# Performance work log

Measured on AMD Instinct MI355X. Metric: run time of the kernel, lower is better.

The kernel has to match this reference:

```python
import jax, jax.numpy as jnp
import numpy as np

B, S, D, H = 4, 2048, 1024, 16
DH = D // H


def setup_inputs() -> dict:
    key = jax.random.key(0)
    ks = jax.random.split(key, 7)
    return {
        "Q": jax.random.normal(ks[0], (B, S, D), dtype=jnp.float32),
        "K": jax.random.normal(ks[1], (B, S, D), dtype=jnp.float32),
        "V": jax.random.normal(ks[2], (B, S, D), dtype=jnp.float32),
        "q_proj": jax.random.normal(ks[3], (D, D), dtype=jnp.float32),
        "k_proj": jax.random.normal(ks[4], (D, D), dtype=jnp.float32),
        "v_proj": jax.random.normal(ks[5], (D, D), dtype=jnp.float32),
        "output_proj": jax.random.normal(ks[6], (D, D), dtype=jnp.float32),
        "casual": 1,
    }


def reference(Q, K, V, q_proj, k_proj, v_proj, output_proj, casual):
    # projections: einsum('... a b, ... s b -> ... s a') == x @ W.T
    q = jnp.einsum('bsd,ad->bsa', Q, q_proj)
    k = jnp.einsum('bsd,ad->bsa', K, k_proj)
    v = jnp.einsum('bsd,ad->bsa', V, v_proj)
    # split heads: [B, S, H, DH]
    q = q.reshape(B, S, H, DH)
    k = k.reshape(B, S, H, DH)
    v = v.reshape(B, S, H, DH)
    # scores [B, H, Sq, Sk]
    scores = jnp.einsum('bqhd,bkhd->bhqk', q, k) / np.sqrt(DH).astype(np.float32)
    # causal mask: 0 on lower triangle, -inf above
    causal_mask = jnp.where(
        jnp.tril(jnp.ones((S, S), dtype=bool)), 0.0, -jnp.inf
    ).astype(scores.dtype)
    scores = scores + causal_mask
    attn = jax.nn.softmax(scores, axis=-1)
    # weighted values -> [B, Sq, H, DH] -> [B, Sq, D]
    out = jnp.einsum('bhqk,bkhd->bqhd', attn, v).reshape(B, S, D)
    # output projection: einsum('... a b, ... b -> ... a') == x @ W.T
    return jnp.einsum('bsd,ad->bsa', out, output_proj)
```

## Files before the change

kernel.cpp:

```cpp
#include <hip/hip_runtime.h>


typedef __attribute__((ext_vector_type(8))) _Float16 half8;
typedef __attribute__((ext_vector_type(4))) float f32x4;

#define DEVI static __device__ __forceinline__

static constexpr int cB = 4, cS = 2048, cD = 1024, cH = 16, cDH = 64;
static constexpr int cM = cB * cS;

DEVI unsigned short h2b(_Float16 h) { union { _Float16 f; unsigned short u; } x; x.f = h; return x.u; }

DEVI void async16(const void* g, void* l) {
#if defined(__HIP_DEVICE_COMPILE__)
  __builtin_amdgcn_global_load_lds((const __attribute__((address_space(1))) unsigned int*)g,
                                   (__attribute__((address_space(3))) unsigned int*)l, 16, 0, 0);
#endif
}

__global__ void split4_kernel(const float* __restrict__ Wq, const float* __restrict__ Wk,
                              const float* __restrict__ Wv, const float* __restrict__ Wo,
                              unsigned short* __restrict__ Wqh, unsigned short* __restrict__ Wql,
                              unsigned short* __restrict__ Wkh, unsigned short* __restrict__ Wkl,
                              unsigned short* __restrict__ Wvh, unsigned short* __restrict__ Woh) {
  const int w = blockIdx.x >> 10, blk = blockIdx.x & 1023;
  const float* in = (w == 0) ? Wq : (w == 1) ? Wk : (w == 2) ? Wv : Wo;
  unsigned short* hi = (w == 0) ? Wqh : (w == 1) ? Wkh : (w == 2) ? Wvh : Woh;
  unsigned short* lo = (w == 0) ? Wql : (w == 1) ? Wkl : nullptr;
  int i = (blk * 256 + (int)threadIdx.x) * 4;
  float4 v = *(const float4*)(in + i);
  _Float16 h0 = (_Float16)v.x, h1 = (_Float16)v.y, h2 = (_Float16)v.z, h3 = (_Float16)v.w;
  unsigned short th[4] = {h2b(h0), h2b(h1), h2b(h2), h2b(h3)};
  *(uint2*)(hi + i) = *(const uint2*)th;
  if (lo != nullptr) {
    unsigned short tl[4] = {h2b((_Float16)(v.x - (float)h0)), h2b((_Float16)(v.y - (float)h1)),
                            h2b((_Float16)(v.z - (float)h2)), h2b((_Float16)(v.w - (float)h3))};
    *(uint2*)(lo + i) = *(const uint2*)tl;
  }
}

__global__ void split_act_kernel(const float* __restrict__ Q, const float* __restrict__ K,
                                 unsigned short* __restrict__ Qh, unsigned short* __restrict__ Ql,
                                 unsigned short* __restrict__ Kh, unsigned short* __restrict__ Kl) {
  const int t = blockIdx.x >> 13;
  const int blk = blockIdx.x & 8191;
  const float* in = t ? K : Q;
  unsigned short* hi = t ? Kh : Qh;
  unsigned short* lo = t ? Kl : Ql;
  int i = (blk * 256 + (int)threadIdx.x) * 4;
  float4 v = *(const float4*)(in + i);
  _Float16 h0 = (_Float16)v.x, h1 = (_Float16)v.y, h2 = (_Float16)v.z, h3 = (_Float16)v.w;
  unsigned short th[4] = {h2b(h0), h2b(h1), h2b(h2), h2b(h3)};
  *(uint2*)(hi + i) = *(const uint2*)th;
  unsigned short tl[4] = {h2b((_Float16)(v.x - (float)h0)), h2b((_Float16)(v.y - (float)h1)),
                          h2b((_Float16)(v.z - (float)h2)), h2b((_Float16)(v.w - (float)h3))};
  *(uint2*)(lo + i) = *(const uint2*)tl;
}

__global__ __launch_bounds__(256, 3) void proj_qk(
    const unsigned short* __restrict__ Qh, const unsigned short* __restrict__ Ql,
    const unsigned short* __restrict__ Kh, const unsigned short* __restrict__ Kl,
    const unsigned short* __restrict__ Wqh, const unsigned short* __restrict__ Wql,
    const unsigned short* __restrict__ Wkh, const unsigned short* __restrict__ Wkl,
    unsigned short* __restrict__ qph, unsigned short* __restrict__ qpl,
    unsigned short* __restrict__ kph, unsigned short* __restrict__ kpl) {
  constexpr int N = cD, K = cD;
  __shared__ unsigned short sAh[128 * 32];
  __shared__ unsigned short sAl[128 * 32];
  __shared__ unsigned short sBh[128 * 32];
  __shared__ unsigned short sBl[128 * 32];

  const int wid = ((int)blockIdx.x & 7) * 128 + ((int)blockIdx.x >> 3);
  const int job = wid >> 9;
  const int bid = wid & 511;
  const unsigned short* Ah_g = job ? Kh : Qh;
  const unsigned short* Al_g = job ? Kl : Ql;
  const unsigned short* Bh = job ? Wkh : Wqh;
  const unsigned short* Bl = job ? Wkl : Wql;
  unsigned short* C0 = job ? kph : qph;
  unsigned short* C1 = job ? kpl : qpl;

  const int tid = threadIdx.x, lane = tid & 63, wave = tid >> 6;
  const int wm = wave >> 1, wn = wave & 1;
  const int bm = bid >> 3, bn = bid & 7;
  const long r0 = (long)bm * 128, c0 = (long)bn * 128;
  const int quad = lane >> 4, cl = lane & 15;
  const int lrow16 = lane >> 2, lg4 = lane & 3;

  f32x4 acc[4][4];
#pragma unroll
  for (int mt = 0; mt < 4; ++mt)
#pragma unroll
    for (int nt = 0; nt < 4; ++nt) acc[mt][nt] = f32x4{0.f, 0.f, 0.f, 0.f};

  for (int k0 = 0; k0 < K; k0 += 32) {
    __syncthreads();
#pragma unroll
    for (int c = 0; c < 2; ++c) {
      int cc = wave * 2 + c;
      int r = cc * 16 + lrow16;
      int sw = (lg4 ^ ((lrow16 >> 1) & 3)) * 8;
      long ga = (r0 + r) * (long)K + k0 + sw;
      long gb = (c0 + r) * (long)K + k0 + sw;
      async16(Ah_g + ga, sAh + cc * 512);
      async16(Al_g + ga, sAl + cc * 512);
      async16(Bh + gb, sBh + cc * 512);
      async16(Bl + gb, sBl + cc * 512);
    }
    __syncthreads();

    half8 ah[4], al[4], bh8[4], bl8[4];
#pragma unroll
    for (int mt = 0; mt < 4; ++mt) {
      int r = wm * 64 + mt * 16 + cl;
      int s = quad ^ ((r >> 1) & 3);
      ah[mt] = *(const half8*)(sAh + r * 32 + s * 8);
      al[mt] = *(const half8*)(sAl + r * 32 + s * 8);
    }
#pragma unroll
    for (int nt = 0; nt < 4; ++nt) {
      int r = wn * 64 + nt * 16 + cl;
      int s = quad ^ ((r >> 1) & 3);
      bh8[nt] = *(const half8*)(sBh + r * 32 + s * 8);
      bl8[nt] = *(const half8*)(sBl + r * 32 + s * 8);
    }
#pragma unroll
    for (int mt = 0; mt < 4; ++mt)
#pragma unroll
      for (int nt = 0; nt < 4; ++nt) {
        acc[mt][nt] = __builtin_amdgcn_mfma_f32_16x16x32_f16(ah[mt], bh8[nt], acc[mt][nt], 0, 0, 0);
        acc[mt][nt] = __builtin_amdgcn_mfma_f32_16x16x32_f16(ah[mt], bl8[nt], acc[mt][nt], 0, 0, 0);
        acc[mt][nt] = __builtin_amdgcn_mfma_f32_16x16x32_f16(al[mt], bh8[nt], acc[mt][nt], 0, 0, 0);
      }
  }

#pragma unroll
  for (int mt = 0; mt < 4; ++mt)
#pragma unroll
    for (int nt = 0; nt < 4; ++nt)
#pragma unroll
      for (int i = 0; i < 4; ++i) {
        long row = r0 + wm * 64 + mt * 16 + quad * 4 + i;
        long col = c0 + wn * 64 + nt * 16 + cl;
        float v = acc[mt][nt][i];
        _Float16 hh = (_Float16)v;
        C0[row * N + col] = h2b(hh);
        C1[row * N + col] = h2b((_Float16)(v - (float)hh));
      }
}

__global__ __launch_bounds__(256, 3) void proj_v(const float* __restrict__ Va,
                                                 const unsigned short* __restrict__ Wvh,
                                                 unsigned short* __restrict__ vp) {
  constexpr int N = cD, K = cD;
  __shared__ float sA32[128 * 32];
  __shared__ unsigned short sBh[128 * 32];

  const int wid = ((int)blockIdx.x & 7) * 64 + ((int)blockIdx.x >> 3);
  const int bm = wid >> 3, bn = wid & 7;
  const long r0 = (long)bm * 128, c0 = (long)bn * 128;

  const int tid = threadIdx.x, lane = tid & 63, wave = tid >> 6;
  const int wm = wave >> 1, wn = wave & 1;
  const int quad = lane >> 4, cl = lane & 15;
  const int lrow8 = lane >> 3, lg8 = lane & 7;
  const int lrow16 = lane >> 2, lg4 = lane & 3;

  f32x4 acc[4][4];
#pragma unroll
  for (int mt = 0; mt < 4; ++mt)
#pragma unroll
    for (int nt = 0; nt < 4; ++nt) acc[mt][nt] = f32x4{0.f, 0.f, 0.f, 0.f};

  for (int k0 = 0; k0 < K; k0 += 32) {
    __syncthreads();
#pragma unroll
    for (int c = 0; c < 4; ++c) {
      int cc = wave * 4 + c;
      int r = cc * 8 + lrow8;
      const float* g = Va + (r0 + r) * (long)K + k0 + ((lg8 ^ lrow8) * 4);
      async16(g, sA32 + cc * 256);
    }
#pragma unroll
    for (int c = 0; c < 2; ++c) {
      int cc = wave * 2 + c;
      int r = cc * 16 + lrow16;
      long gb = (c0 + r) * (long)K + k0 + ((lg4 ^ ((lrow16 >> 1) & 3)) * 8);
      async16(Wvh + gb, sBh + cc * 512);
    }
    __syncthreads();

    half8 ah[4], bh8[4];
#pragma unroll
    for (int mt = 0; mt < 4; ++mt) {
      int r = wm * 64 + mt * 16 + cl;
      int s0 = (quad * 2 + 0) ^ (r & 7), s1 = (quad * 2 + 1) ^ (r & 7);
      float fa[8];
      *(float4*)(fa) = *(const float4*)(sA32 + r * 32 + s0 * 4);
      *(float4*)(fa + 4) = *(const float4*)(sA32 + r * 32 + s1 * 4);
#pragma unroll
      for (int j = 0; j < 8; ++j) ah[mt][j] = (_Float16)fa[j];
    }
#pragma unroll
    for (int nt = 0; nt < 4; ++nt) {
      int r = wn * 64 + nt * 16 + cl;
      int s = quad ^ ((r >> 1) & 3);
      bh8[nt] = *(const half8*)(sBh + r * 32 + s * 8);
    }
#pragma unroll
    for (int mt = 0; mt < 4; ++mt)
#pragma unroll
      for (int nt = 0; nt < 4; ++nt)
        acc[mt][nt] = __builtin_amdgcn_mfma_f32_16x16x32_f16(ah[mt], bh8[nt], acc[mt][nt], 0, 0, 0);
  }

#pragma unroll
  for (int mt = 0; mt < 4; ++mt)
#pragma unroll
    for (int nt = 0; nt < 4; ++nt)
#pragma unroll
      for (int i = 0; i < 4; ++i) {
        long row = r0 + wm * 64 + mt * 16 + quad * 4 + i;
        long col = c0 + wn * 64 + nt * 16 + cl;
        vp[row * N + col] = h2b((_Float16)acc[mt][nt][i]);
      }
}

__global__ __launch_bounds__(256, 2) void gemm_out(const unsigned short* __restrict__ A16p,
                                                   const unsigned short* __restrict__ Bh,
                                                   float* __restrict__ C0, int M, int N, int K) {
  __shared__ unsigned short sA16[128 * 32];
  __shared__ unsigned short sB16[128 * 32];

  const int tid = threadIdx.x, lane = tid & 63, wave = tid >> 6;
  const int wm = wave >> 1, wn = wave & 1;
  const int nb = N >> 7;
  const int wid = ((int)blockIdx.x & 7) * 64 + ((int)blockIdx.x >> 3);
  const int bm = wid / nb, bn = wid % nb;
  const long r0 = (long)bm * 128, c0 = (long)bn * 128;
  const int quad = lane >> 4, cl = lane & 15;
  const int lrow16 = lane >> 2, lg4 = lane & 3;

  f32x4 acc[4][4];
#pragma unroll
  for (int mt = 0; mt < 4; ++mt)
#pragma unroll
    for (int nt = 0; nt < 4; ++nt) acc[mt][nt] = f32x4{0.f, 0.f, 0.f, 0.f};

  for (int k0 = 0; k0 < K; k0 += 32) {
    __syncthreads();
#pragma unroll
    for (int c = 0; c < 2; ++c) {
      int cc = wave * 2 + c;
      int r = cc * 16 + lrow16;
      int sw = (lg4 ^ ((lrow16 >> 1) & 3)) * 8;
      async16(A16p + (r0 + r) * (long)K + k0 + sw, sA16 + cc * 512);
      async16(Bh + (c0 + r) * (long)K + k0 + sw, sB16 + cc * 512);
    }
    __syncthreads();

    half8 ah[4], bh8[4];
#pragma unroll
    for (int mt = 0; mt < 4; ++mt) {
      int r = wm * 64 + mt * 16 + cl;
      int s = quad ^ ((r >> 1) & 3);
      ah[mt] = *(const half8*)(sA16 + r * 32 + s * 8);
    }
#pragma unroll
    for (int nt = 0; nt < 4; ++nt) {
      int r = wn * 64 + nt * 16 + cl;
      int s = quad ^ ((r >> 1) & 3);
      bh8[nt] = *(const half8*)(sB16 + r * 32 + s * 8);
    }
#pragma unroll
    for (int mt = 0; mt < 4; ++mt)
#pragma unroll
      for (int nt = 0; nt < 4; ++nt)
        acc[mt][nt] = __builtin_amdgcn_mfma_f32_16x16x32_f16(ah[mt], bh8[nt], acc[mt][nt], 0, 0, 0);
  }

#pragma unroll
  for (int mt = 0; mt < 4; ++mt)
#pragma unroll
    for (int nt = 0; nt < 4; ++nt)
#pragma unroll
      for (int i = 0; i < 4; ++i) {
        long row = r0 + wm * 64 + mt * 16 + quad * 4 + i;
        long col = c0 + wn * 64 + nt * 16 + cl;
        C0[row * N + col] = acc[mt][nt][i];
      }
}

__global__ __launch_bounds__(256, 3) void flash_kernel(
    const unsigned short* __restrict__ qh_g, const unsigned short* __restrict__ ql_g,
    const unsigned short* __restrict__ kh_g, const unsigned short* __restrict__ kl_g,
    const unsigned short* __restrict__ vp_g, unsigned short* __restrict__ out) {
  __shared__ unsigned short sKh[64 * 64];
  __shared__ unsigned short sKl[64 * 64];
  __shared__ unsigned int sVtU[64 * 34];
  __shared__ unsigned short sP[4][32 * 40];

  const int tid = threadIdx.x, lane = tid & 63, wave = tid >> 6;
  const int quad = lane >> 4, cl = lane & 15;
  const int bh = blockIdx.x & 63;
  const int qt = 15 - (blockIdx.x >> 6);
  const int h = bh & 15;
  const int b = bh >> 4;
  const long rowbase = (long)b * cS;
  const int q0 = qt * 128;
  const int lrow8 = lane >> 3, lg8 = lane & 7;

  half8 qh[2][2], ql[2][2];
  const _Float16 s8 = (_Float16)0.125f;
#pragma unroll
  for (int ks = 0; ks < 2; ++ks)
#pragma unroll
    for (int mt = 0; mt < 2; ++mt) {
      long r = rowbase + q0 + wave * 32 + mt * 16 + cl;
      long off = r * cD + h * 64 + ks * 32 + quad * 8;
      qh[ks][mt] = *(const half8*)(qh_g + off) * s8;
      ql[ks][mt] = *(const half8*)(ql_g + off) * s8;
    }

  f32x4 O[2][5];
  float mrow[2][4];
#pragma unroll
  for (int mt = 0; mt < 2; ++mt) {
#pragma unroll
    for (int dt = 0; dt < 5; ++dt) O[mt][dt] = f32x4{0.f, 0.f, 0.f, 0.f};
#pragma unroll
    for (int i = 0; i < 4; ++i) mrow[mt][i] = -1e30f;
  }

  half8 vone;
#pragma unroll
  for (int j = 0; j < 8; ++j) vone[j] = (cl == 0) ? (_Float16)1.0f : (_Float16)0.0f;

  auto tile = [&](int ki, bool MASK) {
    __syncthreads();
#pragma unroll
    for (int c = 0; c < 2; ++c) {
      int cc = wave * 2 + c;
      int r = cc * 8 + lrow8;
      long g = (rowbase + ki * 64 + r) * (long)cD + h * 64 + ((lg8 ^ lrow8) * 8);
      async16(kh_g + g, sKh + cc * 512);
      async16(kl_g + g, sKl + cc * 512);
    }
    {
      int r2 = tid & 31, dc = (tid >> 5) * 8;
      const unsigned short* gv = vp_g + (rowbase + ki * 64 + 2 * r2) * (long)cD + h * 64 + dc;
      unsigned short a[8], bb[8];
      *(uint4*)a = *(const uint4*)gv;
      *(uint4*)bb = *(const uint4*)(gv + cD);
#pragma unroll
      for (int j = 0; j < 8; ++j)
        sVtU[(dc + j) * 34 + r2] = (unsigned int)a[j] | ((unsigned int)bb[j] << 16);
    }
    __syncthreads();

    f32x4 sacc[2][4];
#pragma unroll
    for (int mt = 0; mt < 2; ++mt)
#pragma unroll
      for (int nt = 0; nt < 4; ++nt) sacc[mt][nt] = f32x4{0.f, 0.f, 0.f, 0.f};
#pragma unroll
    for (int ks = 0; ks < 2; ++ks) {
      half8 kh8[4], kl8[4];
#pragma unroll
      for (int nt = 0; nt < 4; ++nt) {
        int r = nt * 16 + cl;
        int off = r * 64 + (((ks * 4 + quad) ^ (r & 7)) * 8);
        kh8[nt] = *(const half8*)(sKh + off);
        kl8[nt] = *(const half8*)(sKl + off);
      }
#pragma unroll
      for (int mt = 0; mt < 2; ++mt)
#pragma unroll
        for (int nt = 0; nt < 4; ++nt) {
          sacc[mt][nt] = __builtin_amdgcn_mfma_f32_16x16x32_f16(qh[ks][mt], kh8[nt], sacc[mt][nt], 0, 0, 0);
          sacc[mt][nt] = __builtin_amdgcn_mfma_f32_16x16x32_f16(qh[ks][mt], kl8[nt], sacc[mt][nt], 0, 0, 0);
          sacc[mt][nt] = __builtin_amdgcn_mfma_f32_16x16x32_f16(ql[ks][mt], kh8[nt], sacc[mt][nt], 0, 0, 0);
        }
    }
    if (MASK) {
#pragma unroll
      for (int mt = 0; mt < 2; ++mt)
#pragma unroll
        for (int nt = 0; nt < 4; ++nt)
#pragma unroll
          for (int i = 0; i < 4; ++i) {
            int rg = q0 + wave * 32 + mt * 16 + quad * 4 + i;
            int cg = ki * 64 + nt * 16 + cl;
            if (cg > rg) sacc[mt][nt][i] = -1e30f;
          }
    }
    float mnew[2][4];
    bool ch = false;
#pragma unroll
    for (int mt = 0; mt < 2; ++mt)
#pragma unroll
      for (int i = 0; i < 4; ++i) {
        float mx = fmaxf(fmaxf(sacc[mt][0][i], sacc[mt][1][i]),
                         fmaxf(sacc[mt][2][i], sacc[mt][3][i]));
#pragma unroll
        for (int d = 1; d < 16; d <<= 1) mx = fmaxf(mx, __shfl_xor(mx, d));
        ch |= (mx > mrow[mt][i]);
        mnew[mt][i] = fmaxf(mrow[mt][i], mx);
      }
    if (__ballot(ch)) {
#pragma unroll
      for (int mt = 0; mt < 2; ++mt)
#pragma unroll
        for (int i = 0; i < 4; ++i) {
          float a = __expf(mrow[mt][i] - mnew[mt][i]);
#pragma unroll
          for (int dt = 0; dt < 5; ++dt) O[mt][dt][i] *= a;
        }
    }
#pragma unroll
    for (int mt = 0; mt < 2; ++mt)
#pragma unroll
      for (int i = 0; i < 4; ++i) mrow[mt][i] = mnew[mt][i];

    unsigned short* sPw = sP[wave];
#pragma unroll
    for (int kc = 0; kc < 2; ++kc) {
#pragma unroll
      for (int mt = 0; mt < 2; ++mt)
#pragma unroll
        for (int ntl = 0; ntl < 2; ++ntl) {
          int nt = kc * 2 + ntl;
#pragma unroll
          for (int i = 0; i < 4; ++i) {
            float p = __expf(sacc[mt][nt][i] - mrow[mt][i]);
            sPw[(mt * 16 + quad * 4 + i) * 40 + ntl * 16 + cl] = h2b((_Float16)p);
          }
        }
      half8 pa[2], vb[4];
#pragma unroll
      for (int mt = 0; mt < 2; ++mt)
        pa[mt] = *(const half8*)(sPw + (mt * 16 + cl) * 40 + quad * 8);
#pragma unroll
      for (int dt = 0; dt < 4; ++dt) {
        int base = (dt * 16 + cl) * 34 + kc * 16 + quad * 4;
        union { uint4 u; half8 hh; } cvt;
        uint2 p0 = *(const uint2*)(sVtU + base);
        uint2 p1 = *(const uint2*)(sVtU + base + 2);
        cvt.u = uint4{p0.x, p0.y, p1.x, p1.y};
        vb[dt] = cvt.hh;
      }
#pragma unroll
      for (int mt = 0; mt < 2; ++mt) {
#pragma unroll
        for (int dt = 0; dt < 4; ++dt)
          O[mt][dt] = __builtin_amdgcn_mfma_f32_16x16x32_f16(pa[mt], vb[dt], O[mt][dt], 0, 0, 0);
        O[mt][4] = __builtin_amdgcn_mfma_f32_16x16x32_f16(pa[mt], vone, O[mt][4], 0, 0, 0);
      }
    }
  };

  const int full = 2 * qt;
  for (int ki = 0; ki < full; ++ki) tile(ki, false);
  tile(full, true);
  tile(full + 1, true);

  float lv[2][4];
#pragma unroll
  for (int mt = 0; mt < 2; ++mt)
#pragma unroll
    for (int i = 0; i < 4; ++i) lv[mt][i] = __shfl(O[mt][4][i], (lane & 48));
#pragma unroll
  for (int mt = 0; mt < 2; ++mt)
#pragma unroll
    for (int dt = 0; dt < 4; ++dt)
#pragma unroll
      for (int i = 0; i < 4; ++i) {
        long r = rowbase + q0 + wave * 32 + mt * 16 + quad * 4 + i;
        out[r * cD + h * 64 + dt * 16 + cl] = h2b((_Float16)(O[mt][dt][i] / lv[mt][i]));
      }
}

extern "C" void kernel_launch(void* const* d_in, const int* in_sizes, int n_in,
                              void* d_out, int out_size, void* d_ws, size_t ws_size,
                              hipStream_t stream) {
  const float* Q = (const float*)d_in[0];
  const float* K = (const float*)d_in[1];
  const float* V = (const float*)d_in[2];
  const float* Wq = (const float*)d_in[3];
  const float* Wk = (const float*)d_in[4];
  const float* Wv = (const float*)d_in[5];
  const float* Wo = (const float*)d_in[6];

  unsigned short* ws = (unsigned short*)d_ws;
  const size_t WD = (size_t)cD * cD;
  const size_t WM = (size_t)cM * cD;
  unsigned short* Wqh = ws;
  unsigned short* Wql = Wqh + WD;
  unsigned short* Wkh = Wql + WD;
  unsigned short* Wkl = Wkh + WD;
  unsigned short* Wvh = Wkl + WD;
  unsigned short* Woh = Wvh + WD;
  unsigned short* R1 = Woh + WD;
  unsigned short* R2 = R1 + WM;
  unsigned short* qph = R2 + WM;
  unsigned short* qpl = qph + WM;
  unsigned short* kph = qpl + WM;
  unsigned short* kpl = kph + WM;

  unsigned short* Qh = (unsigned short*)d_out;
  unsigned short* Ql = Qh + WM;
  unsigned short* Kh = R1;
  unsigned short* Kl = R2;
  unsigned short* vp = R1;
  unsigned short* attnb = R2;

  split4_kernel<<<4096, 256, 0, stream>>>(Wq, Wk, Wv, Wo, Wqh, Wql, Wkh, Wkl, Wvh, Woh);
  split_act_kernel<<<16384, 256, 0, stream>>>(Q, K, Qh, Ql, Kh, Kl);

  proj_qk<<<1024, 256, 0, stream>>>(Qh, Ql, Kh, Kl, Wqh, Wql, Wkh, Wkl,
                                    qph, qpl, kph, kpl);
  proj_v<<<512, 256, 0, stream>>>(V, Wvh, vp);

  flash_kernel<<<cB * cH * 16, 256, 0, stream>>>(qph, qpl, kph, kpl, vp, attnb);

  const int gblk = (cM / 128) * (cD / 128);
  gemm_out<<<gblk, 256, 0, stream>>>(attnb, Woh, (float*)d_out, cM, cD, cD);
}
```

Measured before the change: 487.6 us.

## Double-buffer K tiles and prefetch V registers in flash attention loop

```diff
diff --git a/kernel.cpp b/kernel.cpp
--- a/kernel.cpp
+++ b/kernel.cpp
@@ -295,8 +295,8 @@
     const unsigned short* __restrict__ qh_g, const unsigned short* __restrict__ ql_g,
     const unsigned short* __restrict__ kh_g, const unsigned short* __restrict__ kl_g,
     const unsigned short* __restrict__ vp_g, unsigned short* __restrict__ out) {
-  __shared__ unsigned short sKh[64 * 64];
-  __shared__ unsigned short sKl[64 * 64];
+  __shared__ unsigned short sKh[2][64 * 64];
+  __shared__ unsigned short sKl[2][64 * 64];
   __shared__ unsigned int sVtU[64 * 34];
   __shared__ unsigned short sP[4][32 * 40];
 
@@ -336,27 +336,49 @@
 #pragma unroll
   for (int j = 0; j < 8; ++j) vone[j] = (cl == 0) ? (_Float16)1.0f : (_Float16)0.0f;
 
-  auto tile = [&](int ki, bool MASK) {
-    __syncthreads();
+  const int r2 = tid & 31, dc = (tid >> 5) * 8;
+  const unsigned short* vbase = vp_g + (rowbase + 2 * r2) * (long)cD + h * 64 + dc;
+
+  auto stageK = [&](int ki, int p) {
 #pragma unroll
     for (int c = 0; c < 2; ++c) {
       int cc = wave * 2 + c;
       int r = cc * 8 + lrow8;
       long g = (rowbase + ki * 64 + r) * (long)cD + h * 64 + ((lg8 ^ lrow8) * 8);
-      async16(kh_g + g, sKh + cc * 512);
-      async16(kl_g + g, sKl + cc * 512);
-    }
+      async16(kh_g + g, &sKh[p][cc * 512]);
+      async16(kl_g + g, &sKl[p][cc * 512]);
+    }
+  };
+  auto loadV = [&](int ki, uint4& v0, uint4& v1) {
+    const unsigned short* gv = vbase + (long)ki * 64 * cD;
+    v0 = *(const uint4*)gv;
+    v1 = *(const uint4*)(gv + cD);
+  };
+
+  const int full = 2 * qt;
+  const int NT = full + 2;
+
+  uint4 cv0, cv1;
+  uint4 nv0 = uint4{0, 0, 0, 0}, nv1 = uint4{0, 0, 0, 0};
+  stageK(0, 0);
+  loadV(0, cv0, cv1);
+
+  auto tile = [&](int ki, bool MASK) {
+    const int p = ki & 1;
+    __syncthreads();
     {
-      int r2 = tid & 31, dc = (tid >> 5) * 8;
-      const unsigned short* gv = vp_g + (rowbase + ki * 64 + 2 * r2) * (long)cD + h * 64 + dc;
       unsigned short a[8], bb[8];
-      *(uint4*)a = *(const uint4*)gv;
-      *(uint4*)bb = *(const uint4*)(gv + cD);
+      *(uint4*)a = cv0;
+      *(uint4*)bb = cv1;
 #pragma unroll
       for (int j = 0; j < 8; ++j)
         sVtU[(dc + j) * 34 + r2] = (unsigned int)a[j] | ((unsigned int)bb[j] << 16);
     }
     __syncthreads();
+    if (ki + 1 < NT) {
+      stageK(ki + 1, p ^ 1);
+      loadV(ki + 1, nv0, nv1);
+    }
 
     f32x4 sacc[2][4];
 #pragma unroll
@@ -370,8 +392,8 @@
       for (int nt = 0; nt < 4; ++nt) {
         int r = nt * 16 + cl;
         int off = r * 64 + (((ks * 4 + quad) ^ (r & 7)) * 8);
-        kh8[nt] = *(const half8*)(sKh + off);
-        kl8[nt] = *(const half8*)(sKl + off);
+        kh8[nt] = *(const half8*)(&sKh[p][off]);
+        kl8[nt] = *(const half8*)(&sKl[p][off]);
       }
 #pragma unroll
       for (int mt = 0; mt < 2; ++mt)
@@ -432,8 +454,8 @@
           int nt = kc * 2 + ntl;
 #pragma unroll
           for (int i = 0; i < 4; ++i) {
-            float p = __expf(sacc[mt][nt][i] - mrow[mt][i]);
-            sPw[(mt * 16 + quad * 4 + i) * 40 + ntl * 16 + cl] = h2b((_Float16)p);
+            float p2 = __expf(sacc[mt][nt][i] - mrow[mt][i]);
+            sPw[(mt * 16 + quad * 4 + i) * 40 + ntl * 16 + cl] = h2b((_Float16)p2);
           }
         }
       half8 pa[2], vb[4];
@@ -457,9 +479,10 @@
         O[mt][4] = __builtin_amdgcn_mfma_f32_16x16x32_f16(pa[mt], vone, O[mt][4], 0, 0, 0);
       }
     }
+    cv0 = nv0;
+    cv1 = nv1;
   };
 
-  const int full = 2 * qt;
   for (int ki = 0; ki < full; ++ki) tile(ki, false);
   tile(full, true);
   tile(full + 1, true);
```

After: 518.3 us. 6.3% more time.
